# Performance work log

Measured on AMD Instinct MI355X. Metric: run time of the kernel, lower is better.

The kernel has to match this reference:

```python
import jax, jax.numpy as jnp
import numpy as np

B, S, D, K = 32, 1024, 256, 1024
DECAY = 0.99
EPS = 1e-05          # EMA laplace epsilon
LN_EPS = 1e-05       # LayerNorm epsilon
COMMITMENT_COST = 0.25


def setup_inputs() -> dict:
    key = jax.random.key(0)
    k1, k2, k3 = jax.random.split(key, 3)
    inputs = jax.random.normal(k1, (B, S, D), jnp.float32)
    # nn.Embedding init: uniform(-1/K, 1/K)
    weight = jax.random.uniform(k2, (K, D), jnp.float32, -1.0 / K, 1.0 / K)
    ema_w = jax.random.normal(k3, (K, D), jnp.float32)
    ema_cluster_size = jnp.zeros((K,), jnp.float32)
    ln_gamma = jnp.ones((D,), jnp.float32)
    ln_beta = jnp.zeros((D,), jnp.float32)
    return {"inputs": inputs, "weight": weight, "ema_w": ema_w,
            "ema_cluster_size": ema_cluster_size,
            "ln_gamma": ln_gamma, "ln_beta": ln_beta}


def _layernorm(x, g, b):
    mu = jnp.mean(x, axis=-1, keepdims=True)
    var = jnp.mean((x - mu) ** 2, axis=-1, keepdims=True)
    return (x - mu) * jax.lax.rsqrt(var + LN_EPS) * g + b


def reference(inputs, weight, ema_w, ema_cluster_size, ln_gamma, ln_beta):
    flat_input = inputs.reshape(-1, D)          # [N, D] (unnormalized, used for EMA dw)
    feats = _layernorm(flat_input, ln_gamma, ln_beta)  # norm_input in sample()

    # euclidean distances ||f||^2 + ||w||^2 - 2 f w^T  -> [N, K]
    d = (jnp.sum(feats ** 2, axis=1, keepdims=True)
         + jnp.sum(weight ** 2, axis=1)
         - 2.0 * feats @ weight.T)

    sampled_dist = jnp.min(d, axis=1)           # [N]
    idx_flat = jnp.argmin(d, axis=1)            # [N] int

    # faithful reproduction of the source's reordering:
    # argsort per batch row (values in [0,S)) then flat-index into the [N]-long index vector
    order = jnp.argsort(sampled_dist.reshape(B, S), axis=1).reshape(-1)  # [N], values in [0,S)
    enc_idx = idx_flat[order]                   # [N]

    quantized = weight[enc_idx].reshape(B, S, D)

    # ---- EMA codebook update (training path), no gradients ----
    fi = jax.lax.stop_gradient(flat_input)
    counts = jax.ops.segment_sum(jnp.ones((B * S,), jnp.float32), enc_idx,
                                 num_segments=K)                    # encodings.sum(0)
    new_cs = ema_cluster_size * DECAY + (1.0 - DECAY) * counts
    n = jnp.sum(new_cs)
    new_cs = (new_cs + EPS) / (n + K * EPS) * n
    dw = jax.ops.segment_sum(fi, enc_idx, num_segments=K)            # encodings.T @ flat_input
    new_ema_w = jax.lax.stop_gradient(ema_w) * DECAY + (1.0 - DECAY) * dw
    new_weight = new_ema_w / new_cs[:, None]

    # ---- losses (avg=False, loss_type=0) ----
    e_latent = jnp.mean((jax.lax.stop_gradient(quantized) - inputs) ** 2)
    q_latent = jnp.mean((quantized - jax.lax.stop_gradient(inputs)) ** 2)
    loss = q_latent + COMMITMENT_COST * e_latent

    # straight-through estimator
    quantized_st = inputs + jax.lax.stop_gradient(quantized - inputs)

    avg_probs = counts / (B * S)
    perplexity = jnp.exp(-jnp.sum(avg_probs * jnp.log(avg_probs + 1e-10)))

    return quantized_st, loss, perplexity, enc_idx, new_weight, new_ema_w, new_cs
```

## Files before the change

### kernel.cpp

```cpp
#include <hip/hip_runtime.h>
#include <cmath>

#define B_ 32
#define S_ 1024
#define D_ 256
#define K_ 1024
#define N_ (B_*S_)

#define O_Q     0
#define O_LOSS  8388608
#define O_PERP  8388609
#define O_IDX   8388610
#define O_NW    8421378
#define O_NEW   8683522
#define O_NCS   8945666

#define OFF_FH    0ull
#define OFF_WH    16777216ull
#define OFF_BW    17301504ull
#define OFF_BWF   17309696ull
#define OFF_SAMP  17313792ull
#define OFF_IDXF  17575936ull
#define OFF_ENC   17707008ull
#define OFF_CNT   17838080ull
#define OFF_SLOWC 17842176ull
#define OFF_SLOWL 17842240ull
#define OFF_LOSSP 17973312ull
#define OFF_COFF  18235456ull
#define OFF_CUR   18239552ull
#define OFF_ROWL  18243648ull

#define MARGIN 4e-5f

typedef _Float16 f16x8 __attribute__((ext_vector_type(8)));
typedef _Float16 f16x4 __attribute__((ext_vector_type(4)));
typedef float    f32x4 __attribute__((ext_vector_type(4)));

#define GL16(gp, lp) __builtin_amdgcn_global_load_lds( \
    (const __attribute__((address_space(1))) unsigned int*)(const void*)(gp), \
    (__attribute__((address_space(3))) unsigned int*)(void*)(lp), 16, 0, 0)

__global__ void k_pre(const float* __restrict__ x, const float* __restrict__ gam,
                      const float* __restrict__ bet, _Float16* __restrict__ fh,
                      const float* __restrict__ w, double* __restrict__ Bw,
                      float* __restrict__ Bwf, _Float16* __restrict__ wh) {
    int lane = threadIdx.x & 63, wv = threadIdx.x >> 6;
    if (blockIdx.x < N_ / 4) {
        int n = blockIdx.x * 4 + wv;
        const float4 xv = ((const float4*)(x + (size_t)n * D_))[lane];
        const float4 gv = ((const float4*)gam)[lane];
        const float4 bv = ((const float4*)bet)[lane];
        float s = xv.x + xv.y + xv.z + xv.w;
        for (int m = 32; m > 0; m >>= 1) s += __shfl_xor(s, m, 64);
        float mu = s * (1.0f / 256.0f);
        float c0 = xv.x - mu, c1 = xv.y - mu, c2 = xv.z - mu, c3 = xv.w - mu;
        float vs = c0 * c0 + c1 * c1 + c2 * c2 + c3 * c3;
        for (int m = 32; m > 0; m >>= 1) vs += __shfl_xor(vs, m, 64);
        float inv = 1.0f / sqrtf(vs * (1.0f / 256.0f) + 1e-5f);
        f16x4 o;
        o[0] = (_Float16)(c0 * inv * gv.x + bv.x);
        o[1] = (_Float16)(c1 * inv * gv.y + bv.y);
        o[2] = (_Float16)(c2 * inv * gv.z + bv.z);
        o[3] = (_Float16)(c3 * inv * gv.w + bv.w);
        *(f16x4*)&fh[(size_t)n * D_ + lane * 4] = o;
    } else {
        int k = (blockIdx.x - N_ / 4) * 4 + wv;
        const float4 v = ((const float4*)(w + (size_t)k * D_))[lane];
        double s = (double)v.x * v.x + (double)v.y * v.y
                 + (double)v.z * v.z + (double)v.w * v.w;
        for (int m = 32; m > 0; m >>= 1) s += __shfl_xor(s, m, 64);
        f16x4 o;
        o[0] = (_Float16)v.x; o[1] = (_Float16)v.y;
        o[2] = (_Float16)v.z; o[3] = (_Float16)v.w;
        *(f16x4*)&wh[(size_t)k * D_ + lane * 4] = o;
        if (lane == 0) { Bw[k] = s; Bwf[k] = (float)s; }
    }
}

__launch_bounds__(512, 4)
__global__ void k_phase1(const _Float16* __restrict__ fh, const _Float16* __restrict__ wh,
                         const float* __restrict__ Bwf, float* __restrict__ pq) {
    __shared__ __align__(16) _Float16 sA[3][128][32];
    __shared__ __align__(16) _Float16 sB[3][256][32];

    const int tid = threadIdx.x;
    const int lane = tid & 63;
    const int w = tid >> 6;
    const int wr = w >> 2;
    const int wc = w & 3;
    const int l15 = lane & 15;
    const int g = lane >> 4;
    const int id = blockIdx.x;
    const int grp = (id & 7) * 32 + (id >> 5);
    const int chunk = (id >> 3) & 3;
    const int row0 = grp * 128;
    const int c0 = chunk * 256;

    const int srow = lane >> 2;
    const int scol = (lane & 3) * 8;
    const _Float16* gp[3];
    int lrow[3]; int isA[3];
#pragma unroll
    for (int j = 0; j < 3; j++) {
        int li = w * 3 + j;
        if (li < 8) {
            isA[j] = 1; lrow[j] = li * 16;
            gp[j] = fh + (size_t)(row0 + li * 16 + srow) * 256 + scol;
        } else {
            isA[j] = 0; lrow[j] = (li - 8) * 16;
            gp[j] = wh + (size_t)(c0 + (li - 8) * 16 + srow) * 256 + scol;
        }
    }

    f32x4 acc[4][4];
#pragma unroll
    for (int a = 0; a < 4; a++)
#pragma unroll
        for (int b = 0; b < 4; b++) acc[a][b] = (f32x4){0.f, 0.f, 0.f, 0.f};

#define STAGE(bi, kk) do { \
    const int eoff_ = (kk) * 32; \
    _Pragma("unroll") \
    for (int j_ = 0; j_ < 3; j_++) { \
        if (isA[j_]) GL16(gp[j_] + eoff_, &sA[bi][lrow[j_]][0]); \
        else         GL16(gp[j_] + eoff_, &sB[bi][lrow[j_]][0]); \
    } \
} while (0)

    STAGE(0, 0);
    STAGE(1, 1);
    asm volatile("s_waitcnt vmcnt(3)" ::: "memory");
    __builtin_amdgcn_s_barrier();
    __builtin_amdgcn_sched_barrier(0);

#pragma unroll
    for (int ks = 0; ks < 8; ks++) {
        const int cur = ks % 3;
        if (ks < 6) STAGE((ks + 2) % 3, ks + 2);

        f16x8 cfr[4];
#pragma unroll
        for (int cb = 0; cb < 4; cb++)
            cfr[cb] = *(const f16x8*)&sB[cur][wc * 64 + cb * 16 + l15][g * 8];
        __builtin_amdgcn_s_setprio(1);
#pragma unroll
        for (int rb = 0; rb < 4; rb++) {
            f16x8 rf = *(const f16x8*)&sA[cur][wr * 64 + rb * 16 + l15][g * 8];
#pragma unroll
            for (int cb = 0; cb < 4; cb++)
                acc[cb][rb] = __builtin_amdgcn_mfma_f32_16x16x32_f16(
                    cfr[cb], rf, acc[cb][rb], 0, 0, 0);
        }
        __builtin_amdgcn_s_setprio(0);
        __builtin_amdgcn_sched_barrier(0);

        if (ks < 6)       asm volatile("s_waitcnt vmcnt(3)" ::: "memory");
        else if (ks == 6) asm volatile("s_waitcnt vmcnt(0)" ::: "memory");
        if (ks < 7) {
            __builtin_amdgcn_s_barrier();
            __builtin_amdgcn_sched_barrier(0);
        }
    }
#undef STAGE
    __syncthreads();

    float bwv[4][4];
#pragma unroll
    for (int cb = 0; cb < 4; cb++)
#pragma unroll
        for (int r = 0; r < 4; r++)
            bwv[cb][r] = Bwf[c0 + wc * 64 + cb * 16 + g * 4 + r];

    float* red = (float*)&sA[0][0][0];
#pragma unroll
    for (int rb = 0; rb < 4; rb++) {
        float m1 = 3e38f, m2 = 3e38f; int c1 = 0x7fffffff;
#pragma unroll
        for (int cb = 0; cb < 4; cb++) {
#pragma unroll
            for (int r = 0; r < 4; r++) {
                float sv = fmaf(-2.0f, acc[cb][rb][r], bwv[cb][r]);
                int c = c0 + wc * 64 + cb * 16 + g * 4 + r;
                if (sv < m1 || (sv == m1 && c < c1)) { m2 = m1; m1 = sv; c1 = c; }
                else if (sv < m2) m2 = sv;
            }
        }
#pragma unroll
        for (int msk = 16; msk <= 32; msk <<= 1) {
            float om1 = __shfl_xor(m1, msk, 64);
            float om2 = __shfl_xor(m2, msk, 64);
            int   oc  = __shfl_xor(c1, msk, 64);
            if (om1 < m1 || (om1 == m1 && oc < c1)) {
                m2 = (m1 < om2) ? m1 : om2; m1 = om1; c1 = oc;
            } else {
                m2 = (om1 < m2) ? om1 : m2;
            }
        }
        if (lane < 16) {
            int rl = wr * 64 + rb * 16 + l15;
            int base = (rl * 4 + wc) * 3;
            red[base] = m1; red[base + 1] = m2; ((int*)red)[base + 2] = c1;
        }
    }
    __syncthreads();
    if (tid < 128) {
        float M1 = 3e38f, M2 = 3e38f; int C1 = 0x7fffffff;
        for (int q = 0; q < 4; q++) {
            int base = (tid * 4 + q) * 3;
            float m1 = red[base], m2 = red[base + 1]; int c = ((int*)red)[base + 2];
            if (m1 < M1 || (m1 == M1 && c < C1)) {
                M2 = (M1 < m2) ? M1 : m2; M1 = m1; C1 = c;
            } else {
                M2 = (m1 < M2) ? m1 : M2;
            }
        }
        pq[chunk * N_ + row0 + tid] = M1;
        pq[4 * N_ + chunk * N_ + row0 + tid] = M2;
        ((int*)pq)[8 * N_ + chunk * N_ + row0 + tid] = C1;
    }
}

__global__ void k_phase2(const float* __restrict__ x, const float* __restrict__ gam,
                         const float* __restrict__ bet, const float* __restrict__ w,
                         const double* __restrict__ Bw, const float* __restrict__ pq,
                         double* __restrict__ sampled, int* __restrict__ idxf,
                         unsigned* __restrict__ slowC, int* __restrict__ slowL) {
    int lane = threadIdx.x & 63, wv = threadIdx.x >> 6;
    int n = blockIdx.x * 4 + wv;
    const float* pm1 = pq;
    const float* pm2 = pq + 4 * N_;
    const int*   pc1 = (const int*)pq + 8 * N_;
    float M1 = 3e38f, M2 = 3e38f; int C1 = 0x7fffffff;
#pragma unroll
    for (int c = 0; c < 4; c++) {
        float m1 = pm1[c * N_ + n], m2 = pm2[c * N_ + n]; int cc = pc1[c * N_ + n];
        if (m1 < M1 || (m1 == M1 && cc < C1)) {
            M2 = (M1 < m2) ? M1 : m2; M1 = m1; C1 = cc;
        } else {
            M2 = (m1 < M2) ? m1 : M2;
        }
    }
    if (M2 - M1 <= MARGIN) {
        if (lane == 0) { unsigned p = atomicAdd(slowC, 1u); slowL[p] = n; }
        return;
    }
    const float* row = x + (size_t)n * D_;
    double xv[4], gv[4], bv[4];
#pragma unroll
    for (int i = 0; i < 4; i++) {
        int d = lane + 64 * i;
        xv[i] = row[d]; gv[i] = gam[d]; bv[i] = bet[d];
    }
    double s = xv[0] + xv[1] + xv[2] + xv[3];
    for (int m = 32; m > 0; m >>= 1) s += __shfl_xor(s, m, 64);
    double mu = s / 256.0, vs = 0.0;
#pragma unroll
    for (int i = 0; i < 4; i++) { double c = xv[i] - mu; vs += c * c; }
    for (int m = 32; m > 0; m >>= 1) vs += __shfl_xor(vs, m, 64);
    double inv = 1.0 / sqrt(vs / 256.0 + 1e-5);
    double f[4], A = 0.0;
#pragma unroll
    for (int i = 0; i < 4; i++) {
        f[i] = (xv[i] - mu) * inv * gv[i] + bv[i];
        A += f[i] * f[i];
    }
    for (int m = 32; m > 0; m >>= 1) A += __shfl_xor(A, m, 64);

    const float* wr_ = w + (size_t)C1 * D_;
    double ss = 0.0;
#pragma unroll
    for (int i = 0; i < 4; i++) ss += f[i] * (double)wr_[lane + 64 * i];
    for (int m = 32; m > 0; m >>= 1) ss += __shfl_xor(ss, m, 64);
    if (lane == 0) { sampled[n] = (A + Bw[C1]) - 2.0 * ss; idxf[n] = C1; }
}

__launch_bounds__(256)
__global__ void k_slow(const float* __restrict__ x, const float* __restrict__ gam,
                       const float* __restrict__ bet, const float* __restrict__ w,
                       const double* __restrict__ Bw,
                       const int* __restrict__ slowL, const unsigned* __restrict__ slowC,
                       double* __restrict__ sampled, int* __restrict__ idxf) {
    __shared__ double sf[256];
    __shared__ double red8[8];
    __shared__ double bmW[4];
    __shared__ int    bcW[4];
    int tid = threadIdx.x, lane = tid & 63, wv = tid >> 6;
    int cnt = (int)*slowC;
    for (int it = blockIdx.x; it < cnt; it += gridDim.x) {
        int n = slowL[it];
        double xv = x[(size_t)n * D_ + tid];
        double gv = gam[tid], bv = bet[tid];
        double s = xv;
        for (int m = 32; m > 0; m >>= 1) s += __shfl_xor(s, m, 64);
        if (lane == 0) red8[wv] = s;
        __syncthreads();
        double mu = (red8[0] + red8[1] + red8[2] + red8[3]) / 256.0;
        double c = xv - mu;
        double v2 = c * c;
        for (int m = 32; m > 0; m >>= 1) v2 += __shfl_xor(v2, m, 64);
        __syncthreads();
        if (lane == 0) red8[wv] = v2;
        __syncthreads();
        double var = (red8[0] + red8[1] + red8[2] + red8[3]) / 256.0;
        double inv = 1.0 / sqrt(var + 1e-5);
        double f = c * inv * gv + bv;
        double a2 = f * f;
        for (int m = 32; m > 0; m >>= 1) a2 += __shfl_xor(a2, m, 64);
        if (lane == 0) red8[4 + wv] = a2;
        sf[tid] = f;
        __syncthreads();
        double A = red8[4] + red8[5] + red8[6] + red8[7];

        double bm = 1.0e300; int bc = 0x7fffffff;
        for (int r = 0; r < 4; r++) {
            int cc = r * 256 + wv * 64 + lane;
            const float* wr = w + (size_t)cc * D_;
            double acc = 0.0;
#pragma unroll 8
            for (int d4 = 0; d4 < 64; d4++) {
                float4 w4 = *(const float4*)(wr + d4 * 4);
                acc += sf[d4 * 4] * (double)w4.x + sf[d4 * 4 + 1] * (double)w4.y
                     + sf[d4 * 4 + 2] * (double)w4.z + sf[d4 * 4 + 3] * (double)w4.w;
            }
            double dist = (A + Bw[cc]) - 2.0 * acc;
            if (dist < bm) { bm = dist; bc = cc; }
        }
        for (int m = 32; m > 0; m >>= 1) {
            double om = __shfl_xor(bm, m, 64);
            int    oc = __shfl_xor(bc, m, 64);
            if (om < bm || (om == bm && oc < bc)) { bm = om; bc = oc; }
        }
        if (lane == 0) { bmW[wv] = bm; bcW[wv] = bc; }
        __syncthreads();
        if (tid == 0) {
            double M = bmW[0]; int C = bcW[0];
            for (int i = 1; i < 4; i++)
                if (bmW[i] < M || (bmW[i] == M && bcW[i] < C)) { M = bmW[i]; C = bcW[i]; }
            sampled[n] = M; idxf[n] = C;
        }
        __syncthreads();
    }
}

__launch_bounds__(1024)
__global__ void k_sort(const double* __restrict__ sampled, const int* __restrict__ idxf,
                       int* __restrict__ enc) {
    __shared__ double val[1024];
    __shared__ int    sid[1024];
    int b = blockIdx.x, t = threadIdx.x;
    val[t] = sampled[(size_t)b * S_ + t];
    sid[t] = t;
    __syncthreads();
    for (int k = 2; k <= 1024; k <<= 1) {
        for (int j = k >> 1; j > 0; j >>= 1) {
            int p = t ^ j;
            if (p > t) {
                double v0 = val[t], v1 = val[p];
                int i0 = sid[t], i1 = sid[p];
                bool gtv = (v0 > v1) || (v0 == v1 && i0 > i1);
                bool asc = ((t & k) == 0);
                if (asc ? gtv : !gtv) {
                    val[t] = v1; val[p] = v0; sid[t] = i1; sid[p] = i0;
                }
            }
            __syncthreads();
        }
    }
    enc[(size_t)b * S_ + t] = idxf[sid[t]];
}

__global__ void k_gather(const float* __restrict__ x, const float* __restrict__ w,
                         const int* __restrict__ enc, float* __restrict__ out,
                         unsigned* __restrict__ cnt, double* __restrict__ lossP) {
    int lane = threadIdx.x & 63, wv = threadIdx.x >> 6;
    int n = blockIdx.x * 4 + wv;
    int e = enc[n];
    const float4 q4 = ((const float4*)(w + (size_t)e * D_))[lane];
    const float4 x4 = ((const float4*)(x + (size_t)n * D_))[lane];
    ((float4*)(out + O_Q + (size_t)n * D_))[lane] = q4;
    double d0 = (double)q4.x - (double)x4.x;
    double d1 = (double)q4.y - (double)x4.y;
    double d2 = (double)q4.z - (double)x4.z;
    double d3 = (double)q4.w - (double)x4.w;
    double ls = d0 * d0 + d1 * d1 + d2 * d2 + d3 * d3;
    for (int m = 32; m > 0; m >>= 1) ls += __shfl_xor(ls, m, 64);
    if (lane == 0) {
        lossP[n] = ls;
        out[O_IDX + n] = (float)e;
        atomicAdd(&cnt[e], 1u);
    }
}

__launch_bounds__(1024)
__global__ void k_scan(const unsigned* __restrict__ cnt, int* __restrict__ coff,
                       int* __restrict__ cur) {
    __shared__ int tmp[1024];
    int t = threadIdx.x;
    int my = (int)cnt[t];
    tmp[t] = my;
    __syncthreads();
    for (int off = 1; off < 1024; off <<= 1) {
        int v = (t >= off) ? tmp[t - off] : 0;
        __syncthreads();
        tmp[t] += v;
        __syncthreads();
    }
    int excl = tmp[t] - my;
    coff[t] = excl;
    cur[t] = excl;
}

__global__ void k_scatter(const int* __restrict__ enc, int* __restrict__ cur,
                          int* __restrict__ rowl) {
    int n = blockIdx.x * 256 + threadIdx.x;
    int e = enc[n];
    int p = atomicAdd(&cur[e], 1);
    rowl[p] = n;
}

__launch_bounds__(256)
__global__ void k_post(const unsigned* __restrict__ cnt, const float* __restrict__ ema_cs,
                       const double* __restrict__ lossP,
                       const int* __restrict__ coff, const int* __restrict__ rowl,
                       const float* __restrict__ x, const float* __restrict__ ema_w,
                       float* __restrict__ out) {
    __shared__ double redd[24];
    __shared__ double ntot_s;
    int tid = threadIdx.x;

    double part = 0.0;
    for (int i = tid; i < K_; i += 256)
        part += (double)(0.99f * ema_cs[i] + 0.01f * (float)cnt[i]);
    for (int m = 32; m > 0; m >>= 1) part += __shfl_xor(part, m, 64);
    if ((tid & 63) == 0) redd[tid >> 6] = part;
    __syncthreads();
    if (tid == 0) ntot_s = redd[0] + redd[1] + redd[2] + redd[3];
    __syncthreads();
    double ntot = ntot_s;

    if (blockIdx.x < K_) {
        int k = blockIdx.x;
        float cs0 = 0.99f * ema_cs[k] + 0.01f * (float)cnt[k];
        double csf = ((double)cs0 + 1e-5) / (ntot + 1024.0 * 1e-5) * ntot;
        int base = coff[k];
        int c = (int)cnt[k];
        float acc = 0.0f;
        int j = 0;
        for (; j + 4 <= c; j += 4) {
            int r0 = rowl[base + j];
            int r1 = rowl[base + j + 1];
            int r2 = rowl[base + j + 2];
            int r3 = rowl[base + j + 3];
            float v0 = x[(size_t)r0 * D_ + tid];
            float v1 = x[(size_t)r1 * D_ + tid];
            float v2 = x[(size_t)r2 * D_ + tid];
            float v3 = x[(size_t)r3 * D_ + tid];
            acc += v0; acc += v1; acc += v2; acc += v3;
        }
        for (; j < c; j++) acc += x[(size_t)rowl[base + j] * D_ + tid];
        size_t idx = (size_t)k * D_ + tid;
        float ne = 0.99f * ema_w[idx] + 0.01f * acc;
        out[O_NEW + idx] = ne;
        out[O_NW + idx] = ne / (float)csf;
    } else {
        for (int i = tid; i < K_; i += 256) {
            float cs0 = 0.99f * ema_cs[i] + 0.01f * (float)cnt[i];
            double c2 = ((double)cs0 + 1e-5) / (ntot + 1024.0 * 1e-5) * ntot;
            out[O_NCS + i] = (float)c2;
        }
        double ent = 0.0;
        for (int i = tid; i < K_; i += 256) {
            double p = (double)cnt[i] / 32768.0;
            ent += -p * log(p + 1e-10);
        }
        for (int m = 32; m > 0; m >>= 1) ent += __shfl_xor(ent, m, 64);
        if ((tid & 63) == 0) redd[8 + (tid >> 6)] = ent;
        double ls = 0.0;
        for (int i = tid; i < N_; i += 256) ls += lossP[i];
        for (int m = 32; m > 0; m >>= 1) ls += __shfl_xor(ls, m, 64);
        if ((tid & 63) == 0) redd[16 + (tid >> 6)] = ls;
        __syncthreads();
        if (tid == 0) {
            double e = redd[8] + redd[9] + redd[10] + redd[11];
            double l = redd[16] + redd[17] + redd[18] + redd[19];
            out[O_PERP] = (float)exp(e);
            out[O_LOSS] = (float)(1.25 * l / 8388608.0);
        }
    }
}

extern "C" void kernel_launch(void* const* d_in, const int* in_sizes, int n_in,
                              void* d_out, int out_size, void* d_ws, size_t ws_size,
                              hipStream_t stream) {
    (void)in_sizes; (void)n_in; (void)out_size; (void)ws_size;
    const float* x      = (const float*)d_in[0];
    const float* w      = (const float*)d_in[1];
    const float* ema_w  = (const float*)d_in[2];
    const float* ema_cs = (const float*)d_in[3];
    const float* g      = (const float*)d_in[4];
    const float* bt     = (const float*)d_in[5];
    float* out = (float*)d_out;
    char* ws = (char*)d_ws;

    _Float16* fh = (_Float16*)(ws + OFF_FH);
    _Float16* wh = (_Float16*)(ws + OFF_WH);
    double* Bw   = (double*)(ws + OFF_BW);
    float*  Bwf  = (float*)(ws + OFF_BWF);
    double* samp = (double*)(ws + OFF_SAMP);
    int*    idxf = (int*)(ws + OFF_IDXF);
    int*    enc  = (int*)(ws + OFF_ENC);
    unsigned* cnt = (unsigned*)(ws + OFF_CNT);
    unsigned* slowC = (unsigned*)(ws + OFF_SLOWC);
    int*    slowL = (int*)(ws + OFF_SLOWL);
    double* lossP = (double*)(ws + OFF_LOSSP);
    int*    coff  = (int*)(ws + OFF_COFF);
    int*    cur   = (int*)(ws + OFF_CUR);
    int*    rowl  = (int*)(ws + OFF_ROWL);

    (void)hipMemsetAsync(ws + OFF_CNT, 0, 4160, stream);

    k_pre<<<N_ / 4 + K_ / 4, 256, 0, stream>>>(x, g, bt, fh, w, Bw, Bwf, wh);
    k_phase1<<<1024, 512, 0, stream>>>(fh, wh, Bwf, out);
    k_phase2<<<N_ / 4, 256, 0, stream>>>(x, g, bt, w, Bw, out, samp, idxf, slowC, slowL);
    k_slow<<<2048, 256, 0, stream>>>(x, g, bt, w, Bw, slowL, slowC, samp, idxf);
    k_sort<<<B_, 1024, 0, stream>>>(samp, idxf, enc);
    k_gather<<<N_ / 4, 256, 0, stream>>>(x, w, enc, out, cnt, lossP);
    k_scan<<<1, 1024, 0, stream>>>(cnt, coff, cur);
    k_scatter<<<N_ / 256, 256, 0, stream>>>(enc, cur, rowl);
    k_post<<<K_ + 1, 256, 0, stream>>>(cnt, ema_cs, lossP, coff, rowl, x, ema_w, out);
}
```

Measured before the change: 272.7 us.

## Shrink phase1 GEMM tiles to 128x128 with double buffering; slim sort block

The distance GEMM kernel moves from 512-thread blocks computing 128x256 tiles with a triple-buffered LDS pipeline to 256-thread blocks computing 128x128 tiles with double buffering, across twice as many blocks. The partial-min buffers grow from 4 column chunks to 8, and phase2 merges 8 partials per row. The bitonic sort kernel now uses 256 threads that each handle 4 elements instead of 1024 threads. This trades less LDS per block and possibly higher occupancy for lower per-block reuse of the A tile, a shallower prefetch with a full vmcnt(0) wait every step, and extra partial-result traffic.

```diff
diff --git a/kernel.cpp b/kernel.cpp
--- a/kernel.cpp
+++ b/kernel.cpp
@@ -77,37 +77,38 @@
     }
 }
 
-__launch_bounds__(512, 4)
+__launch_bounds__(256, 4)
 __global__ void k_phase1(const _Float16* __restrict__ fh, const _Float16* __restrict__ wh,
                          const float* __restrict__ Bwf, float* __restrict__ pq) {
-    __shared__ __align__(16) _Float16 sA[3][128][32];
-    __shared__ __align__(16) _Float16 sB[3][256][32];
+    __shared__ __align__(16) _Float16 sA[2][128][32];
+    __shared__ __align__(16) _Float16 sB[2][128][32];
 
     const int tid = threadIdx.x;
     const int lane = tid & 63;
     const int w = tid >> 6;
-    const int wr = w >> 2;
-    const int wc = w & 3;
+    const int wr = w >> 1;
+    const int wc = w & 1;
     const int l15 = lane & 15;
     const int g = lane >> 4;
     const int id = blockIdx.x;
-    const int grp = (id & 7) * 32 + (id >> 5);
-    const int chunk = (id >> 3) & 3;
+    const int grp = (id & 7) * 32 + (id >> 6);
+    const int chunk = (id >> 3) & 7;
     const int row0 = grp * 128;
-    const int c0 = chunk * 256;
+    const int c0 = chunk * 128;
 
     const int srow = lane >> 2;
     const int scol = (lane & 3) * 8;
-    const _Float16* gp[3];
-    int lrow[3]; int isA[3];
-#pragma unroll
-    for (int j = 0; j < 3; j++) {
-        int li = w * 3 + j;
-        if (li < 8) {
-            isA[j] = 1; lrow[j] = li * 16;
+    const bool isA = (w < 2);
+    const _Float16* gp[4];
+    int lrow[4];
+#pragma unroll
+    for (int j = 0; j < 4; j++) {
+        int li = w * 4 + j;
+        if (isA) {
+            lrow[j] = li * 16;
             gp[j] = fh + (size_t)(row0 + li * 16 + srow) * 256 + scol;
         } else {
-            isA[j] = 0; lrow[j] = (li - 8) * 16;
+            lrow[j] = (li - 8) * 16;
             gp[j] = wh + (size_t)(c0 + (li - 8) * 16 + srow) * 256 + scol;
         }
     }
@@ -121,22 +122,21 @@
 #define STAGE(bi, kk) do { \
     const int eoff_ = (kk) * 32; \
     _Pragma("unroll") \
-    for (int j_ = 0; j_ < 3; j_++) { \
-        if (isA[j_]) GL16(gp[j_] + eoff_, &sA[bi][lrow[j_]][0]); \
-        else         GL16(gp[j_] + eoff_, &sB[bi][lrow[j_]][0]); \
+    for (int j_ = 0; j_ < 4; j_++) { \
+        if (isA) GL16(gp[j_] + eoff_, &sA[bi][lrow[j_]][0]); \
+        else     GL16(gp[j_] + eoff_, &sB[bi][lrow[j_]][0]); \
     } \
 } while (0)
 
     STAGE(0, 0);
-    STAGE(1, 1);
-    asm volatile("s_waitcnt vmcnt(3)" ::: "memory");
+    asm volatile("s_waitcnt vmcnt(0)" ::: "memory");
     __builtin_amdgcn_s_barrier();
     __builtin_amdgcn_sched_barrier(0);
 
 #pragma unroll
     for (int ks = 0; ks < 8; ks++) {
-        const int cur = ks % 3;
-        if (ks < 6) STAGE((ks + 2) % 3, ks + 2);
+        const int cur = ks & 1;
+        if (ks < 7) STAGE(cur ^ 1, ks + 1);
 
         f16x8 cfr[4];
 #pragma unroll
@@ -154,9 +154,8 @@
         __builtin_amdgcn_s_setprio(0);
         __builtin_amdgcn_sched_barrier(0);
 
-        if (ks < 6)       asm volatile("s_waitcnt vmcnt(3)" ::: "memory");
-        else if (ks == 6) asm volatile("s_waitcnt vmcnt(0)" ::: "memory");
         if (ks < 7) {
+            asm volatile("s_waitcnt vmcnt(0)" ::: "memory");
             __builtin_amdgcn_s_barrier();
             __builtin_amdgcn_sched_barrier(0);
         }
@@ -198,15 +197,15 @@
         }
         if (lane < 16) {
             int rl = wr * 64 + rb * 16 + l15;
-            int base = (rl * 4 + wc) * 3;
+            int base = (rl * 2 + wc) * 3;
             red[base] = m1; red[base + 1] = m2; ((int*)red)[base + 2] = c1;
         }
     }
     __syncthreads();
     if (tid < 128) {
         float M1 = 3e38f, M2 = 3e38f; int C1 = 0x7fffffff;
-        for (int q = 0; q < 4; q++) {
-            int base = (tid * 4 + q) * 3;
+        for (int q = 0; q < 2; q++) {
+            int base = (tid * 2 + q) * 3;
             float m1 = red[base], m2 = red[base + 1]; int c = ((int*)red)[base + 2];
             if (m1 < M1 || (m1 == M1 && c < C1)) {
                 M2 = (M1 < m2) ? M1 : m2; M1 = m1; C1 = c;
@@ -215,8 +214,8 @@
             }
         }
         pq[chunk * N_ + row0 + tid] = M1;
-        pq[4 * N_ + chunk * N_ + row0 + tid] = M2;
-        ((int*)pq)[8 * N_ + chunk * N_ + row0 + tid] = C1;
+        pq[8 * N_ + chunk * N_ + row0 + tid] = M2;
+        ((int*)pq)[16 * N_ + chunk * N_ + row0 + tid] = C1;
     }
 }
 
@@ -228,11 +227,11 @@
     int lane = threadIdx.x & 63, wv = threadIdx.x >> 6;
     int n = blockIdx.x * 4 + wv;
     const float* pm1 = pq;
-    const float* pm2 = pq + 4 * N_;
-    const int*   pc1 = (const int*)pq + 8 * N_;
+    const float* pm2 = pq + 8 * N_;
+    const int*   pc1 = (const int*)pq + 16 * N_;
     float M1 = 3e38f, M2 = 3e38f; int C1 = 0x7fffffff;
 #pragma unroll
-    for (int c = 0; c < 4; c++) {
+    for (int c = 0; c < 8; c++) {
         float m1 = pm1[c * N_ + n], m2 = pm2[c * N_ + n]; int cc = pc1[c * N_ + n];
         if (m1 < M1 || (m1 == M1 && cc < C1)) {
             M2 = (M1 < m2) ? M1 : m2; M1 = m1; C1 = cc;
@@ -342,31 +341,43 @@
     }
 }
 
-__launch_bounds__(1024)
+__launch_bounds__(256)
 __global__ void k_sort(const double* __restrict__ sampled, const int* __restrict__ idxf,
                        int* __restrict__ enc) {
     __shared__ double val[1024];
     __shared__ int    sid[1024];
     int b = blockIdx.x, t = threadIdx.x;
-    val[t] = sampled[(size_t)b * S_ + t];
-    sid[t] = t;
+#pragma unroll
+    for (int e = 0; e < 4; e++) {
+        int i = t + e * 256;
+        val[i] = sampled[(size_t)b * S_ + i];
+        sid[i] = i;
+    }
     __syncthreads();
     for (int k = 2; k <= 1024; k <<= 1) {
         for (int j = k >> 1; j > 0; j >>= 1) {
-            int p = t ^ j;
-            if (p > t) {
-                double v0 = val[t], v1 = val[p];
-                int i0 = sid[t], i1 = sid[p];
-                bool gtv = (v0 > v1) || (v0 == v1 && i0 > i1);
-                bool asc = ((t & k) == 0);
-                if (asc ? gtv : !gtv) {
-                    val[t] = v1; val[p] = v0; sid[t] = i1; sid[p] = i0;
+#pragma unroll
+            for (int e = 0; e < 4; e++) {
+                int i = t + e * 256;
+                int p = i ^ j;
+                if (p > i) {
+                    double v0 = val[i], v1 = val[p];
+                    int i0 = sid[i], i1 = sid[p];
+                    bool gtv = (v0 > v1) || (v0 == v1 && i0 > i1);
+                    bool asc = ((i & k) == 0);
+                    if (asc ? gtv : !gtv) {
+                        val[i] = v1; val[p] = v0; sid[i] = i1; sid[p] = i0;
+                    }
                 }
             }
             __syncthreads();
         }
     }
-    enc[(size_t)b * S_ + t] = idxf[sid[t]];
+#pragma unroll
+    for (int e = 0; e < 4; e++) {
+        int i = t + e * 256;
+        enc[(size_t)b * S_ + i] = idxf[sid[i]];
+    }
 }
 
 __global__ void k_gather(const float* __restrict__ x, const float* __restrict__ w,
@@ -520,10 +531,10 @@
     (void)hipMemsetAsync(ws + OFF_CNT, 0, 4160, stream);
 
     k_pre<<<N_ / 4 + K_ / 4, 256, 0, stream>>>(x, g, bt, fh, w, Bw, Bwf, wh);
-    k_phase1<<<1024, 512, 0, stream>>>(fh, wh, Bwf, out);
+    k_phase1<<<2048, 256, 0, stream>>>(fh, wh, Bwf, out);
     k_phase2<<<N_ / 4, 256, 0, stream>>>(x, g, bt, w, Bw, out, samp, idxf, slowC, slowL);
     k_slow<<<2048, 256, 0, stream>>>(x, g, bt, w, Bw, slowL, slowC, samp, idxf);
-    k_sort<<<B_, 1024, 0, stream>>>(samp, idxf, enc);
+    k_sort<<<B_, 256, 0, stream>>>(samp, idxf, enc);
     k_gather<<<N_ / 4, 256, 0, stream>>>(x, w, enc, out, cnt, lossP);
     k_scan<<<1, 1024, 0, stream>>>(cnt, coff, cur);
     k_scatter<<<N_ / 256, 256, 0, stream>>>(enc, cur, rowl);
```

Measured after the change: 292.2 us. 1.07x slower.

## Replace per-batch bitonic sort with parallel rank-counting sort

Applied to the files above, without the earlier changes.

Replaces the single-block-per-batch bitonic sort with a rank-by-counting kernel. Each thread computes the sorted position of one element by comparing it against all 1024 values in shared memory, breaking ties by index. It then scatters the codebook index straight to that position. This removes the 55 barrier-separated bitonic stages and spreads the work over four times as many blocks. In exchange each element does O(S) comparisons, giving quadratic total work.

```diff
diff --git a/kernel.cpp b/kernel.cpp
--- a/kernel.cpp
+++ b/kernel.cpp
@@ -342,31 +342,27 @@
     }
 }
 
-__launch_bounds__(1024)
-__global__ void k_sort(const double* __restrict__ sampled, const int* __restrict__ idxf,
+__launch_bounds__(256)
+__global__ void k_rank(const double* __restrict__ sampled, const int* __restrict__ idxf,
                        int* __restrict__ enc) {
     __shared__ double val[1024];
-    __shared__ int    sid[1024];
-    int b = blockIdx.x, t = threadIdx.x;
-    val[t] = sampled[(size_t)b * S_ + t];
-    sid[t] = t;
+    int b = blockIdx.x >> 2;
+    int q = blockIdx.x & 3;
+    int t = threadIdx.x;
+    size_t base = (size_t)b * S_;
+#pragma unroll
+    for (int e = 0; e < 4; e++)
+        val[t + e * 256] = sampled[base + t + e * 256];
     __syncthreads();
-    for (int k = 2; k <= 1024; k <<= 1) {
-        for (int j = k >> 1; j > 0; j >>= 1) {
-            int p = t ^ j;
-            if (p > t) {
-                double v0 = val[t], v1 = val[p];
-                int i0 = sid[t], i1 = sid[p];
-                bool gtv = (v0 > v1) || (v0 == v1 && i0 > i1);
-                bool asc = ((t & k) == 0);
-                if (asc ? gtv : !gtv) {
-                    val[t] = v1; val[p] = v0; sid[t] = i1; sid[p] = i0;
-                }
-            }
-            __syncthreads();
-        }
-    }
-    enc[(size_t)b * S_ + t] = idxf[sid[t]];
+    int i = q * 256 + t;
+    double vi = val[i];
+    int rank = 0;
+#pragma unroll 8
+    for (int j = 0; j < 1024; j++) {
+        double vj = val[j];
+        rank += (vj < vi) || (vj == vi && j < i);
+    }
+    enc[base + rank] = idxf[i];
 }
 
 __global__ void k_gather(const float* __restrict__ x, const float* __restrict__ w,
@@ -523,7 +519,7 @@
     k_phase1<<<1024, 512, 0, stream>>>(fh, wh, Bwf, out);
     k_phase2<<<N_ / 4, 256, 0, stream>>>(x, g, bt, w, Bw, out, samp, idxf, slowC, slowL);
     k_slow<<<2048, 256, 0, stream>>>(x, g, bt, w, Bw, slowL, slowC, samp, idxf);
-    k_sort<<<B_, 1024, 0, stream>>>(samp, idxf, enc);
+    k_rank<<<B_ * 4, 256, 0, stream>>>(samp, idxf, enc);
     k_gather<<<N_ / 4, 256, 0, stream>>>(x, w, enc, out, cnt, lossP);
     k_scan<<<1, 1024, 0, stream>>>(cnt, coff, cur);
     k_scatter<<<N_ / 256, 256, 0, stream>>>(enc, cur, rowl);
```

Measured after the change: 281.6 us. 3.3% more time.
